# Kernel optimization log

Measured on AMD Instinct MI355X. Metric: run time of the kernel, lower is better.

The kernel has to match this reference:

```python
import jax, jax.numpy as jnp
import numpy as np

KERAS_EPSILON = 1e-7  # keras.backend.epsilon()


def setup_inputs() -> dict:
    key = jax.random.key(0)
    x = jax.random.normal(key, (4, 2048, 128), dtype=jnp.float32)
    return {"x": x}


def reference(x) -> jnp.ndarray:
    # Euclidean distance matrix: D[b, i, j] = sqrt(sum_d (x[b,i,d] - x[b,j,d])^2 + eps)
    # Computed via the ||a||^2 + ||b||^2 - 2 a.b identity to avoid the
    # [B, N, N, D] broadcasted intermediate of the original implementation.
    sq = jnp.sum(x * x, axis=-1)                      # [B, N]
    cross = jnp.einsum("bnd,bmd->bnm", x, x)           # [B, N, N]
    d2 = sq[:, :, None] + sq[:, None, :] - 2.0 * cross  # [B, N, N]
    d2 = jnp.maximum(d2, 0.0)  # clamp tiny negative rounding errors
    return jnp.sqrt(d2 + KERAS_EPSILON)
```

## Files before the change

kernel.cpp:

```cpp
#include <hip/hip_runtime.h>
#include <hip/hip_bf16.h>

typedef __attribute__((ext_vector_type(8))) __bf16 bf16x8;
typedef __attribute__((ext_vector_type(4))) float  f32x4;

constexpr int NN   = 2048;
constexpr int DD   = 128;
constexpr int TI   = 128;
constexpr int TJ   = 64;
constexpr int LDSS = 136;

__global__ __launch_bounds__(256, 2)
void edm_kernel(const float* __restrict__ x, float* __restrict__ out) {
    __shared__ __align__(16) __bf16 As[TI * LDSS];
    __shared__ __align__(16) __bf16 Bs[TJ * LDSS];
    __shared__ float sqA[TI];
    __shared__ float sqB[TJ];

    const int t  = threadIdx.x;
    const int jt = blockIdx.x;
    const int it = blockIdx.y;
    const int b  = blockIdx.z;

    const float* xb = x + (size_t)b * NN * DD;

    {
        const float* src = xb + (size_t)it * TI * DD;
        #pragma unroll
        for (int iter = 0; iter < 8; ++iter) {
            const int idx = t + iter * 256;
            const int row = idx >> 4;
            const int c16 = idx & 15;
            const float4* p = (const float4*)(src + row * DD + c16 * 8);
            const float4 v0 = p[0];
            const float4 v1 = p[1];
            bf16x8 w;
            w[0] = (__bf16)v0.x; w[1] = (__bf16)v0.y;
            w[2] = (__bf16)v0.z; w[3] = (__bf16)v0.w;
            w[4] = (__bf16)v1.x; w[5] = (__bf16)v1.y;
            w[6] = (__bf16)v1.z; w[7] = (__bf16)v1.w;
            *(bf16x8*)&As[row * LDSS + c16 * 8] = w;
        }
        const float* srcB = xb + (size_t)jt * TJ * DD;
        #pragma unroll
        for (int iter = 0; iter < 4; ++iter) {
            const int idx = t + iter * 256;
            const int row = idx >> 4;
            const int c16 = idx & 15;
            const float4* p = (const float4*)(srcB + row * DD + c16 * 8);
            const float4 v0 = p[0];
            const float4 v1 = p[1];
            bf16x8 w;
            w[0] = (__bf16)v0.x; w[1] = (__bf16)v0.y;
            w[2] = (__bf16)v0.z; w[3] = (__bf16)v0.w;
            w[4] = (__bf16)v1.x; w[5] = (__bf16)v1.y;
            w[6] = (__bf16)v1.z; w[7] = (__bf16)v1.w;
            *(bf16x8*)&Bs[row * LDSS + c16 * 8] = w;
        }
    }
    __syncthreads();

    if (t < TI + TJ) {
        const __bf16* r = (t < TI) ? &As[t * LDSS] : &Bs[(t - TI) * LDSS];
        float s = 0.f;
        #pragma unroll
        for (int k = 0; k < DD; k += 8) {
            bf16x8 v = *(const bf16x8*)(r + k);
            #pragma unroll
            for (int j = 0; j < 8; ++j) { const float f = (float)v[j]; s += f * f; }
        }
        if (t < TI) sqA[t] = s; else sqB[t - TI] = s;
    }
    __syncthreads();

    const int wave = t >> 6;
    const int lane = t & 63;
    const int wm = (wave >> 1) * 64;
    const int wn = (wave & 1) * 32;
    const int lm = lane & 15;
    const int q  = lane >> 4;

    f32x4 acc[4][2] = {};
    #pragma unroll
    for (int ks = 0; ks < 4; ++ks) {
        const int kb = ks * 32 + q * 8;
        bf16x8 a[4], bb[2];
        #pragma unroll
        for (int mf = 0; mf < 4; ++mf)
            a[mf] = *(const bf16x8*)&As[(wm + mf * 16 + lm) * LDSS + kb];
        #pragma unroll
        for (int nf = 0; nf < 2; ++nf)
            bb[nf] = *(const bf16x8*)&Bs[(wn + nf * 16 + lm) * LDSS + kb];
        #pragma unroll
        for (int mf = 0; mf < 4; ++mf)
            #pragma unroll
            for (int nf = 0; nf < 2; ++nf)
                acc[mf][nf] = __builtin_amdgcn_mfma_f32_16x16x32_bf16(
                    a[mf], bb[nf], acc[mf][nf], 0, 0, 0);
    }

    float* outp = out + ((size_t)b * NN + (size_t)it * TI) * NN + (size_t)jt * TJ;
    #pragma unroll
    for (int mf = 0; mf < 4; ++mf) {
        #pragma unroll
        for (int nf = 0; nf < 2; ++nf) {
            const int col = wn + nf * 16 + lm;
            const float sj = sqB[col];
            #pragma unroll
            for (int r = 0; r < 4; ++r) {
                const int row = wm + mf * 16 + q * 4 + r;
                float d2 = sqA[row] + sj - 2.0f * acc[mf][nf][r];
                d2 = fmaxf(d2, 0.0f);
                outp[(size_t)row * NN + col] = sqrtf(d2 + 1e-7f);
            }
        }
    }
}

extern "C" void kernel_launch(void* const* d_in, const int* in_sizes, int n_in,
                              void* d_out, int out_size, void* d_ws, size_t ws_size,
                              hipStream_t stream) {
    const float* x = (const float*)d_in[0];
    float* out = (float*)d_out;
    dim3 grid(NN / TJ, NN / TI, 4);
    edm_kernel<<<grid, dim3(256), 0, stream>>>(x, out);
}
```

Baseline: 86.90 us.

## Split norm kernel, load MFMA operands from global, stage output via LDS for coalesced stores

Squared norms move into a separate small kernel that writes them to workspace, using a wave shuffle reduction. The main kernel drops the shared-memory operand tiles and loads bf16-converted fragments straight from global memory into registers. It enlarges the per-block tile to 128x128, with each wave computing 64x64. The epilogue goes through a padded per-wave LDS tile so each row is written with 16-byte vector stores. This targets scattered scalar output writes and the block barriers, at the cost of redundant global loads per wave and an extra kernel launch.

Measured after the change: 111.2 us. 27.9% more time.

```diff
diff --git a/kernel.cpp b/kernel.cpp
--- a/kernel.cpp
+++ b/kernel.cpp
@@ -4,34 +4,53 @@
 typedef __attribute__((ext_vector_type(8))) __bf16 bf16x8;
 typedef __attribute__((ext_vector_type(4))) float  f32x4;
 
-constexpr int NN   = 2048;
-constexpr int DD   = 128;
-constexpr int TI   = 128;
-constexpr int TJ   = 64;
-constexpr int LDSS = 136;
+constexpr int NN = 2048;
+constexpr int DD = 128;
+constexpr int TS = 65;
 
-__global__ __launch_bounds__(256, 2)
-void edm_kernel(const float* __restrict__ x, float* __restrict__ out) {
-    __shared__ __align__(16) __bf16 As[TI * LDSS];
-    __shared__ __align__(16) __bf16 Bs[TJ * LDSS];
-    __shared__ float sqA[TI];
-    __shared__ float sqB[TJ];
+__global__ __launch_bounds__(256, 4)
+void sq_kernel(const float* __restrict__ x, float* __restrict__ sq) {
+    const int lane = threadIdx.x & 63;
+    const int row  = blockIdx.x * 4 + (threadIdx.x >> 6);
+    const float2 v = *(const float2*)(x + (size_t)row * DD + lane * 2);
+    const float f0 = (float)(__bf16)v.x;
+    const float f1 = (float)(__bf16)v.y;
+    float s = f0 * f0 + f1 * f1;
+    #pragma unroll
+    for (int m = 1; m < 64; m <<= 1) s += __shfl_xor(s, m, 64);
+    if (lane == 0) sq[row] = s;
+}
 
-    const int t  = threadIdx.x;
+__global__ __launch_bounds__(256, 3)
+void edm_main(const float* __restrict__ x, const float* __restrict__ sq,
+              float* __restrict__ out) {
+    __shared__ float tile[4][32 * TS];
+
+    const int t    = threadIdx.x;
+    const int wave = t >> 6;
+    const int lane = t & 63;
+    const int lm   = lane & 15;
+    const int q    = lane >> 4;
+
     const int jt = blockIdx.x;
     const int it = blockIdx.y;
     const int b  = blockIdx.z;
 
-    const float* xb = x + (size_t)b * NN * DD;
+    const int i0 = it * 128 + (wave >> 1) * 64;
+    const int j0 = jt * 128 + (wave & 1) * 64;
 
-    {
-        const float* src = xb + (size_t)it * TI * DD;
+    const float* xb  = x  + (size_t)b * NN * DD;
+    const float* sqb = sq + (size_t)b * NN;
+
+    f32x4 acc[4][4] = {};
+
+    #pragma unroll
+    for (int ks = 0; ks < 4; ++ks) {
+        const int kb = ks * 32 + q * 8;
+        bf16x8 a[4], bb[4];
         #pragma unroll
-        for (int iter = 0; iter < 8; ++iter) {
-            const int idx = t + iter * 256;
-            const int row = idx >> 4;
-            const int c16 = idx & 15;
-            const float4* p = (const float4*)(src + row * DD + c16 * 8);
+        for (int mf = 0; mf < 4; ++mf) {
+            const float4* p = (const float4*)(xb + (size_t)(i0 + mf * 16 + lm) * DD + kb);
             const float4 v0 = p[0];
             const float4 v1 = p[1];
             bf16x8 w;
@@ -39,15 +58,11 @@
             w[2] = (__bf16)v0.z; w[3] = (__bf16)v0.w;
             w[4] = (__bf16)v1.x; w[5] = (__bf16)v1.y;
             w[6] = (__bf16)v1.z; w[7] = (__bf16)v1.w;
-            *(bf16x8*)&As[row * LDSS + c16 * 8] = w;
+            a[mf] = w;
         }
-        const float* srcB = xb + (size_t)jt * TJ * DD;
         #pragma unroll
-        for (int iter = 0; iter < 4; ++iter) {
-            const int idx = t + iter * 256;
-            const int row = idx >> 4;
-            const int c16 = idx & 15;
-            const float4* p = (const float4*)(srcB + row * DD + c16 * 8);
+        for (int nf = 0; nf < 4; ++nf) {
+            const float4* p = (const float4*)(xb + (size_t)(j0 + nf * 16 + lm) * DD + kb);
             const float4 v0 = p[0];
             const float4 v1 = p[1];
             bf16x8 w;
@@ -55,64 +70,48 @@
             w[2] = (__bf16)v0.z; w[3] = (__bf16)v0.w;
             w[4] = (__bf16)v1.x; w[5] = (__bf16)v1.y;
             w[6] = (__bf16)v1.z; w[7] = (__bf16)v1.w;
-            *(bf16x8*)&Bs[row * LDSS + c16 * 8] = w;
+            bb[nf] = w;
         }
-    }
-    __syncthreads();
-
-    if (t < TI + TJ) {
-        const __bf16* r = (t < TI) ? &As[t * LDSS] : &Bs[(t - TI) * LDSS];
-        float s = 0.f;
-        #pragma unroll
-        for (int k = 0; k < DD; k += 8) {
-            bf16x8 v = *(const bf16x8*)(r + k);
-            #pragma unroll
-            for (int j = 0; j < 8; ++j) { const float f = (float)v[j]; s += f * f; }
-        }
-        if (t < TI) sqA[t] = s; else sqB[t - TI] = s;
-    }
-    __syncthreads();
-
-    const int wave = t >> 6;
-    const int lane = t & 63;
-    const int wm = (wave >> 1) * 64;
-    const int wn = (wave & 1) * 32;
-    const int lm = lane & 15;
-    const int q  = lane >> 4;
-
-    f32x4 acc[4][2] = {};
-    #pragma unroll
-    for (int ks = 0; ks < 4; ++ks) {
-        const int kb = ks * 32 + q * 8;
-        bf16x8 a[4], bb[2];
-        #pragma unroll
-        for (int mf = 0; mf < 4; ++mf)
-            a[mf] = *(const bf16x8*)&As[(wm + mf * 16 + lm) * LDSS + kb];
-        #pragma unroll
-        for (int nf = 0; nf < 2; ++nf)
-            bb[nf] = *(const bf16x8*)&Bs[(wn + nf * 16 + lm) * LDSS + kb];
         #pragma unroll
         for (int mf = 0; mf < 4; ++mf)
             #pragma unroll
-            for (int nf = 0; nf < 2; ++nf)
+            for (int nf = 0; nf < 4; ++nf)
                 acc[mf][nf] = __builtin_amdgcn_mfma_f32_16x16x32_bf16(
                     a[mf], bb[nf], acc[mf][nf], 0, 0, 0);
     }
 
-    float* outp = out + ((size_t)b * NN + (size_t)it * TI) * NN + (size_t)jt * TJ;
+    f32x4 sqi[4];
+    float sqj[4];
     #pragma unroll
-    for (int mf = 0; mf < 4; ++mf) {
+    for (int mf = 0; mf < 4; ++mf)
+        sqi[mf] = *(const f32x4*)(sqb + i0 + mf * 16 + q * 4);
+    #pragma unroll
+    for (int nf = 0; nf < 4; ++nf)
+        sqj[nf] = sqb[j0 + nf * 16 + lm];
+
+    float* tl = tile[wave];
+    #pragma unroll
+    for (int h = 0; h < 2; ++h) {
         #pragma unroll
-        for (int nf = 0; nf < 2; ++nf) {
-            const int col = wn + nf * 16 + lm;
-            const float sj = sqB[col];
+        for (int mf2 = 0; mf2 < 2; ++mf2) {
+            const int mf = h * 2 + mf2;
             #pragma unroll
-            for (int r = 0; r < 4; ++r) {
-                const int row = wm + mf * 16 + q * 4 + r;
-                float d2 = sqA[row] + sj - 2.0f * acc[mf][nf][r];
-                d2 = fmaxf(d2, 0.0f);
-                outp[(size_t)row * NN + col] = sqrtf(d2 + 1e-7f);
+            for (int nf = 0; nf < 4; ++nf) {
+                #pragma unroll
+                for (int r = 0; r < 4; ++r) {
+                    float d2 = sqi[mf][r] + sqj[nf] - 2.0f * acc[mf][nf][r];
+                    d2 = fmaxf(d2, 0.0f);
+                    tl[(mf2 * 16 + q * 4 + r) * TS + nf * 16 + lm] = sqrtf(d2 + 1e-7f);
+                }
             }
+        }
+        #pragma unroll
+        for (int iter = 0; iter < 8; ++iter) {
+            const int rr = iter * 4 + q;
+            f32x4 v;
+            #pragma unroll
+            for (int d = 0; d < 4; ++d) v[d] = tl[rr * TS + lm * 4 + d];
+            *(f32x4*)(out + ((size_t)b * NN + i0 + h * 32 + rr) * NN + j0 + lm * 4) = v;
         }
     }
 }
@@ -122,6 +121,8 @@
                               hipStream_t stream) {
     const float* x = (const float*)d_in[0];
     float* out = (float*)d_out;
-    dim3 grid(NN / TJ, NN / TI, 4);
-    edm_kernel<<<grid, dim3(256), 0, stream>>>(x, out);
+    float* sq  = (float*)d_ws;
+
+    sq_kernel<<<dim3(4 * NN / 4), dim3(256), 0, stream>>>(x, sq);
+    edm_main<<<dim3(16, 16, 4), dim3(256), 0, stream>>>(x, sq, out);
 }
```
